# Kernel optimization log

Hardware: AMD Instinct MI355X
Metric: run time of the kernel (lower is better)

## Reference

```python
import jax, jax.numpy as jnp
import numpy as np
import math

EPS = 1e-6
NUM_HEADS = 8


def _layernorm(x, g, b):
    mu = jnp.mean(x, axis=-1, keepdims=True)
    var = jnp.mean(jnp.square(x - mu), axis=-1, keepdims=True)
    return (x - mu) * jax.lax.rsqrt(var + EPS) * g + b


def _pos_embed(n, d):
    pos = jnp.arange(n, dtype=jnp.float32)[:, None]                  # [N,1]
    div = jnp.exp(jnp.arange(0, d, 2, dtype=jnp.float32) * (-math.log(10000.0) / d))
    ang = pos * div                                                  # [N,d/2]
    pe = jnp.stack([jnp.sin(ang), jnp.cos(ang)], axis=-1).reshape(n, d)
    return pe


def setup_inputs() -> dict:
    key = jax.random.key(0)
    B, N, C, L = 2, 2048, 256, 4
    ks = jax.random.split(key, 6)
    s = 0.02
    return {
        "x": jax.random.normal(ks[0], (B, N, C), jnp.float32),
        "qkv_w": jax.random.normal(ks[1], (L, C, 3 * C), jnp.float32) * s,
        "proj_w": jax.random.normal(ks[2], (L, C, C), jnp.float32) * s,
        "proj_b": jnp.zeros((L, C), jnp.float32),
        "w1": jax.random.normal(ks[3], (L, C, C), jnp.float32) * s,
        "b1": jnp.zeros((L, C), jnp.float32),
        "w2": jax.random.normal(ks[4], (L, C, C), jnp.float32) * s,
        "b2": jnp.zeros((L, C), jnp.float32),
        "g1": jnp.ones((L, C), jnp.float32),
        "be1": jnp.zeros((L, C), jnp.float32),
        "g2": jnp.ones((L, C), jnp.float32),
        "be2": jnp.zeros((L, C), jnp.float32),
    }


def reference(x, qkv_w, proj_w, proj_b, w1, b1, w2, b2, g1, be1, g2, be2):
    B, N, C = x.shape
    L = qkv_w.shape[0]
    H = NUM_HEADS
    dh = C // H
    scale = dh ** -0.5

    x = x + _pos_embed(N, C)[None]

    for l in range(L):
        # --- attention (manual QKV, post-norm residual as in source) ---
        qkv = (x @ qkv_w[l]).reshape(B, N, 3, H, dh)
        q, k, v = qkv[:, :, 0], qkv[:, :, 1], qkv[:, :, 2]           # [B,N,H,dh]
        attn = jnp.einsum('bqhd,bkhd->bhqk', q, k) * scale           # [B,H,N,N]
        attn = jax.nn.softmax(attn, axis=-1)
        o = jnp.einsum('bhqk,bkhd->bqhd', attn, v).reshape(B, N, C)
        o = o @ proj_w[l] + proj_b[l]
        x = _layernorm(x + o, g1[l], be1[l])
        # --- MLP (GELU exact, as torch nn.GELU default) ---
        m = jax.nn.gelu(x @ w1[l] + b1[l], approximate=False) @ w2[l] + b2[l]
        x = _layernorm(x + m, g2[l], be2[l])
    return x
```

## Files before the change

kernel.cpp:

```cpp
#include <hip/hip_runtime.h>
#include <math.h>

#define Bd 2
#define Nd 2048
#define Cd 256
#define Ld 4
#define Hd 8
#define Md (Bd*Nd)
#define BHd 16
#define U32d 1024
#define SPLITd 4

typedef __attribute__((ext_vector_type(8))) short bf16x8;
typedef __attribute__((ext_vector_type(4))) float f32x4;
typedef __attribute__((ext_vector_type(16))) float f32x16;
typedef __attribute__((ext_vector_type(4))) short shortx4;

static __device__ inline f32x4 mfma16(bf16x8 a, bf16x8 b, f32x4 c) {
    return __builtin_amdgcn_mfma_f32_16x16x32_bf16(a, b, c, 0, 0, 0);
}
static __device__ inline f32x16 mfma32(bf16x8 a, bf16x8 b, f32x16 c) {
    return __builtin_amdgcn_mfma_f32_32x32x16_bf16(a, b, c, 0, 0, 0);
}
static __device__ inline short f2bf(float f) {
    union { float f; unsigned u; } v; v.f = f;
    unsigned r = (v.u + 0x7fff + ((v.u >> 16) & 1)) >> 16;
    return (short)r;
}
static __device__ inline unsigned pkbf(float a, float b) {
    unsigned r;
    asm("v_cvt_pk_bf16_f32 %0, %1, %2" : "=v"(r) : "v"(a), "v"(b));
    return r;
}
static __device__ inline float bf2f(unsigned u) {
    return __uint_as_float((u & 0xffffu) << 16);
}

__global__ __launch_bounds__(256)
void prep_kernel(const float* __restrict__ x_in, const float* __restrict__ qkv_w,
                 const float* __restrict__ proj_w, const float* __restrict__ w1,
                 const float* __restrict__ w2, float* __restrict__ xf,
                 short* __restrict__ xb, short* __restrict__ qkvT,
                 short* __restrict__ projT, short* __restrict__ w1T,
                 short* __restrict__ w2T, float qscale)
{
    __shared__ float tile[32][33];
    int id = blockIdx.x;
    if (id < 1536) {
        const float* src; short* dst; int Nc; float scale; int lim; int rem; int l;
        if (id < 768)       { l = id / 192;         rem = id % 192; src = qkv_w;  dst = qkvT;  Nc = 768; scale = qscale; lim = 256; }
        else if (id < 1024) { l = (id - 768) / 64;  rem = (id - 768) % 64;  src = proj_w; dst = projT; Nc = 256; scale = 1.f; lim = 0; }
        else if (id < 1280) { l = (id - 1024) / 64; rem = (id - 1024) % 64; src = w1;     dst = w1T;   Nc = 256; scale = 1.f; lim = 0; }
        else                { l = (id - 1280) / 64; rem = (id - 1280) % 64; src = w2;     dst = w2T;   Nc = 256; scale = 1.f; lim = 0; }
        int nb = Nc >> 5;
        int c0 = (rem % nb) * 32, k0 = (rem / nb) * 32;
        src += (size_t)l * 256 * Nc;
        dst += (size_t)l * Nc * 256;
        int tx = threadIdx.x & 31, ty = threadIdx.x >> 5;
#pragma unroll
        for (int i = 0; i < 4; i++) {
            int k = ty + 8 * i;
            tile[k][tx] = src[(size_t)(k0 + k) * Nc + c0 + tx];
        }
        __syncthreads();
#pragma unroll
        for (int i = 0; i < 4; i++) {
            int cc = ty + 8 * i;
            int col = c0 + cc;
            float v = tile[tx][cc];
            if (col < lim) v *= scale;
            dst[(size_t)col * 256 + k0 + tx] = f2bf(v);
        }
    } else {
        int i = (id - 1536) * 256 + threadIdx.x;
        int c = i & (Cd - 1);
        int n = (i >> 8) & (Nd - 1);
        const float kneg = -9.210340371976184f / 256.0f;
        float div = __expf((float)(c & ~1) * kneg);
        float ang = (float)n * div;
        float pe = (c & 1) ? cosf(ang) : sinf(ang);
        float v = x_in[i] + pe;
        xf[i] = v;
        xb[i] = f2bf(v);
    }
}

__global__ __launch_bounds__(256)
void qkv_gemm_kernel(const short* __restrict__ Ab, const short* __restrict__ WT,
                     short* __restrict__ Qh, short* __restrict__ Kh,
                     short* __restrict__ Vtb)
{
    int t = threadIdx.x, w = t >> 6, l = t & 63, c = l & 15, g = l >> 4;
    int rowBase = blockIdx.y * 128 + w * 32;
    int colBase = blockIdx.x * 32;
    const f32x4 zero = {0.f, 0.f, 0.f, 0.f};
    f32x4 acc[2][2] = {{zero, zero}, {zero, zero}};
    const short* ap0 = Ab + (size_t)(rowBase + c) * 256 + g * 8;
    const short* ap1 = ap0 + 16 * 256;
    const short* bp0 = WT + (size_t)(colBase + c) * 256 + g * 8;
    const short* bp1 = bp0 + 16 * 256;
#pragma unroll
    for (int kc = 0; kc < 256; kc += 32) {
        bf16x8 a0 = *(const bf16x8*)(ap0 + kc);
        bf16x8 a1 = *(const bf16x8*)(ap1 + kc);
        bf16x8 b0 = *(const bf16x8*)(bp0 + kc);
        bf16x8 b1 = *(const bf16x8*)(bp1 + kc);
        acc[0][0] = mfma16(a0, b0, acc[0][0]);
        acc[0][1] = mfma16(a0, b1, acc[0][1]);
        acc[1][0] = mfma16(a1, b0, acc[1][0]);
        acc[1][1] = mfma16(a1, b1, acc[1][1]);
    }
    int region = colBase >> 8;
    if (region < 2) {
        short* dst = (region == 0) ? Qh : Kh;
        int cb = colBase - region * 256;
#pragma unroll
        for (int m = 0; m < 2; m++)
#pragma unroll
            for (int n = 0; n < 2; n++) {
                int col = cb + 16 * n + c;
                int h = col >> 5, dh = col & 31;
#pragma unroll
                for (int r = 0; r < 4; r++) {
                    int tok = rowBase + 16 * m + 4 * g + r;
                    int b = tok >> 11, nt = tok & (Nd - 1);
                    dst[((size_t)(b * Hd + h) * Nd + nt) * 32 + dh] = f2bf(acc[m][n][r]);
                }
            }
    } else {
        int b = rowBase >> 11;
        int ntok0 = (rowBase & (Nd - 1)) + 4 * g;
#pragma unroll
        for (int m = 0; m < 2; m++)
#pragma unroll
            for (int n = 0; n < 2; n++) {
                int chg = colBase - 512 + 16 * n + c;
                shortx4 pkv;
#pragma unroll
                for (int r = 0; r < 4; r++) pkv[r] = f2bf(acc[m][n][r]);
                *(shortx4*)&Vtb[(size_t)((b * Hd + (chg >> 5)) * 32 + (chg & 31)) * Nd
                                + ntok0 + 16 * m] = pkv;
            }
    }
}

__global__ __launch_bounds__(512)
void attn_part_kernel(const short* __restrict__ Qh, const short* __restrict__ Kh,
                      const short* __restrict__ Vtb, unsigned* __restrict__ OPb,
                      float* __restrict__ Lsum)
{
    __shared__ short Ks[2][128 * 40];
    __shared__ short Vs[2][32 * 136];

    int t = threadIdx.x, w = t >> 6, l = t & 63;
    int l5 = l >> 5, q32 = l & 31;
    int bid = blockIdx.x;
    int xcd = bid & 7, j = bid >> 3;
    int grp = xcd * 8 + (j >> 3);
    int qt = (j & 7) * 8 + w;
    int part = grp >> 4, bh = grp & 15;

    bool isK = (t < 256);
    int t2 = t & 255;
    int koff = (t2 >> 1) * 40 + (t2 & 1) * 16;
    int voff = (t2 >> 3) * 136 + (t2 & 7) * 16;
    int soff = isK ? koff : voff;
    long sstep = isK ? 128 * 32 : 128;

    const int kstart = part * (Nd / SPLITd);
    const short* sg = isK
        ? Kh + ((size_t)bh * Nd + kstart + (t2 >> 1)) * 32 + (t2 & 1) * 16
        : Vtb + ((size_t)bh * 32 + (t2 >> 3)) * Nd + kstart + (t2 & 7) * 16;

    bf16x8 qf0, qf1;
    {
        const short* qp = Qh + ((size_t)bh * Nd + qt * 32 + q32) * 32 + 8 * l5;
        qf0 = *(const bf16x8*)qp;
        qf1 = *(const bf16x8*)(qp + 16);
    }

    f32x16 O;
#pragma unroll
    for (int i = 0; i < 16; i++) O[i] = 0.f;
    float lsum = 0.f;

    {
        bf16x8 r0 = *(const bf16x8*)sg;
        bf16x8 r1 = *(const bf16x8*)(sg + 8);
        short* d = (isK ? Ks[0] : Vs[0]) + soff;
        *(bf16x8*)d = r0;
        *(bf16x8*)(d + 8) = r1;
    }
    __syncthreads();

    const int NT = (Nd / SPLITd) / 128;
    int cur = 0;
    for (int it = 0; it < NT; ++it) {
        bool has_next = (it + 1) < NT;
        bf16x8 nxt0, nxt1;
        if (has_next) {
            sg += sstep;
            nxt0 = *(const bf16x8*)sg;
            nxt1 = *(const bf16x8*)(sg + 8);
        }

        __builtin_amdgcn_s_setprio(1);
#pragma unroll
        for (int sb = 0; sb < 4; sb++) {
            bf16x8 kf0 = *(const bf16x8*)&Ks[cur][(32 * sb + q32) * 40 + 8 * l5];
            bf16x8 kf1 = *(const bf16x8*)&Ks[cur][(32 * sb + q32) * 40 + 8 * l5 + 16];
            f32x16 s;
#pragma unroll
            for (int i = 0; i < 16; i++) s[i] = 0.f;
            s = mfma32(kf0, qf0, s);
            s = mfma32(kf1, qf1, s);
            float e[16];
#pragma unroll
            for (int i = 0; i < 16; i++) e[i] = exp2f(s[i]);
            float p0 = e[0] + e[1],  p1 = e[2] + e[3];
            float p2 = e[4] + e[5],  p3 = e[6] + e[7];
            float p4 = e[8] + e[9],  p5 = e[10] + e[11];
            float p6 = e[12] + e[13], p7 = e[14] + e[15];
            p0 += p1; p2 += p3; p4 += p5; p6 += p7;
            p0 += p2; p4 += p6;
            lsum += p0 + p4;
            unsigned wd[8];
#pragma unroll
            for (int i = 0; i < 8; i++) wd[i] = pkbf(e[2 * i], e[2 * i + 1]);
#pragma unroll
            for (int half = 0; half < 2; half++) {
                unsigned a0 = wd[4 * half], a1 = wd[4 * half + 1];
                unsigned b0 = wd[4 * half + 2], b1 = wd[4 * half + 3];
                asm("v_permlane32_swap_b32 %0, %1" : "+v"(a0), "+v"(b0));
                asm("v_permlane32_swap_b32 %0, %1" : "+v"(a1), "+v"(b1));
                union { unsigned u[4]; bf16x8 v; } pa;
                pa.u[0] = a0; pa.u[1] = a1; pa.u[2] = b0; pa.u[3] = b1;
                bf16x8 vvf = *(const bf16x8*)&Vs[cur][q32 * 136 + 8 * l5 + 16 * (2 * sb + half)];
                O = mfma32(pa.v, vvf, O);
            }
        }
        __builtin_amdgcn_s_setprio(0);

        if (has_next) {
            short* d = (isK ? Ks[cur ^ 1] : Vs[cur ^ 1]) + soff;
            *(bf16x8*)d = nxt0;
            *(bf16x8*)(d + 8) = nxt1;
            __syncthreads();
            cur ^= 1;
        }
    }

    lsum += __shfl_xor(lsum, 32, 64);

    int u = bh * 64 + qt;
    unsigned* opb = OPb + ((size_t)part * U32d + u) * 512;
#pragma unroll
    for (int i = 0; i < 16; i += 2) {
        int q = (i & 3) + 8 * (i >> 2) + 4 * l5;
        opb[(q >> 1) * 32 + q32] = pkbf(O[i], O[i + 1]);
    }
    if (l5 == 0) Lsum[((size_t)part * U32d + u) * 32 + q32] = lsum;
}

template<int LAST>
__global__ __launch_bounds__(512)
void tail_kernel(const unsigned* __restrict__ OPb, const float* __restrict__ Lsum,
                 const short* __restrict__ WT, const float* __restrict__ bias,
                 const float* __restrict__ resid,
                 const float* __restrict__ g1v, const float* __restrict__ be1v,
                 const short* __restrict__ W1T, const float* __restrict__ b1v,
                 const short* __restrict__ W2T, const float* __restrict__ b2v,
                 const float* __restrict__ g2v, const float* __restrict__ be2v,
                 float* __restrict__ outf, short* __restrict__ outb)
{
    __shared__ short Atile[16 * 264];
    __shared__ short A1[16 * 264];
    __shared__ short A2[16 * 264];
    __shared__ float red[8][16][2];
    int t = threadIdx.x;
    int rowBase = blockIdx.x * 16;

    {
        int r = t >> 5, seg = t & 31;
        int grow = rowBase + r;
        int bb = grow >> 11;
        int qt = (grow & (Nd - 1)) >> 5;
        int q = grow & 31;
        int h = seg >> 2;
        int dh0 = (seg & 3) * 8;
        int u = (bb * Hd + h) * 64 + qt;
        int sh = (q & 1) * 16;
        float o[8] = {0.f, 0.f, 0.f, 0.f, 0.f, 0.f, 0.f, 0.f};
        float L = 0.f;
#pragma unroll
        for (int p = 0; p < SPLITd; p++) {
            const unsigned* src = OPb + ((size_t)p * U32d + u) * 512 + (q >> 1) * 32 + dh0;
            uint4 w0 = *(const uint4*)src;
            uint4 w1 = *(const uint4*)(src + 4);
            o[0] += bf2f(w0.x >> sh); o[1] += bf2f(w0.y >> sh);
            o[2] += bf2f(w0.z >> sh); o[3] += bf2f(w0.w >> sh);
            o[4] += bf2f(w1.x >> sh); o[5] += bf2f(w1.y >> sh);
            o[6] += bf2f(w1.z >> sh); o[7] += bf2f(w1.w >> sh);
            L += Lsum[((size_t)p * U32d + u) * 32 + q];
        }
        float inv = 1.f / L;
        bf16x8 pk;
#pragma unroll
        for (int j = 0; j < 8; j++) pk[j] = f2bf(o[j] * inv);
        *(bf16x8*)&Atile[r * 264 + seg * 8] = pk;
    }
    __syncthreads();

    int w = t >> 6, l = t & 63, c = l & 15, g = l >> 4;
    const f32x4 zero = {0.f, 0.f, 0.f, 0.f};
    int col0 = w * 32 + c, col1 = col0 + 16;

    f32x4 acc0 = zero, acc1 = zero;
    {
        const short* bp0 = WT + (size_t)col0 * 256 + g * 8;
        const short* bp1 = WT + (size_t)col1 * 256 + g * 8;
#pragma unroll
        for (int kc = 0; kc < 256; kc += 32) {
            bf16x8 a = *(const bf16x8*)&Atile[c * 264 + g * 8 + kc];
            acc0 = mfma16(a, *(const bf16x8*)(bp0 + kc), acc0);
            acc1 = mfma16(a, *(const bf16x8*)(bp1 + kc), acc1);
        }
    }

    float vv[2][4], s_[4] = {0.f, 0.f, 0.f, 0.f}, sq_[4] = {0.f, 0.f, 0.f, 0.f};
    {
        float bi0 = bias[col0], bi1 = bias[col1];
#pragma unroll
        for (int r = 0; r < 4; r++) {
            int row = rowBase + 4 * g + r;
            float v0 = acc0[r] + bi0 + resid[(size_t)row * 256 + col0];
            float v1 = acc1[r] + bi1 + resid[(size_t)row * 256 + col1];
            vv[0][r] = v0; vv[1][r] = v1;
            s_[r] += v0 + v1; sq_[r] += v0 * v0 + v1 * v1;
        }
    }
#pragma unroll
    for (int off = 1; off <= 8; off <<= 1)
#pragma unroll
        for (int r = 0; r < 4; r++) {
            s_[r] += __shfl_xor(s_[r], off, 64);
            sq_[r] += __shfl_xor(sq_[r], off, 64);
        }
    if (c == 0)
#pragma unroll
        for (int r = 0; r < 4; r++) {
            red[w][4 * g + r][0] = s_[r];
            red[w][4 * g + r][1] = sq_[r];
        }
    __syncthreads();
    float ln1[2][4];
    {
        float mu[4], rs[4];
#pragma unroll
        for (int r = 0; r < 4; r++) {
            float S = 0.f, Q = 0.f;
#pragma unroll
            for (int ww = 0; ww < 8; ww++) { S += red[ww][4 * g + r][0]; Q += red[ww][4 * g + r][1]; }
            mu[r] = S * (1.f / 256.f);
            rs[r] = rsqrtf(Q * (1.f / 256.f) - mu[r] * mu[r] + 1e-6f);
        }
        float gv0 = g1v[col0], bv0 = be1v[col0], gv1 = g1v[col1], bv1 = be1v[col1];
#pragma unroll
        for (int r = 0; r < 4; r++) {
            float o0 = (vv[0][r] - mu[r]) * rs[r] * gv0 + bv0;
            float o1 = (vv[1][r] - mu[r]) * rs[r] * gv1 + bv1;
            ln1[0][r] = o0; ln1[1][r] = o1;
            A1[(4 * g + r) * 264 + col0] = f2bf(o0);
            A1[(4 * g + r) * 264 + col1] = f2bf(o1);
        }
    }
    __syncthreads();

    {
        f32x4 a0 = zero, a1 = zero;
        const short* bp0 = W1T + (size_t)col0 * 256 + g * 8;
        const short* bp1 = W1T + (size_t)col1 * 256 + g * 8;
#pragma unroll
        for (int kc = 0; kc < 256; kc += 32) {
            bf16x8 a = *(const bf16x8*)&A1[c * 264 + g * 8 + kc];
            a0 = mfma16(a, *(const bf16x8*)(bp0 + kc), a0);
            a1 = mfma16(a, *(const bf16x8*)(bp1 + kc), a1);
        }
        float bi0 = b1v[col0], bi1 = b1v[col1];
#pragma unroll
        for (int r = 0; r < 4; r++) {
            float v0 = a0[r] + bi0, v1 = a1[r] + bi1;
            v0 = 0.5f * v0 * (1.f + erff(v0 * 0.7071067811865476f));
            v1 = 0.5f * v1 * (1.f + erff(v1 * 0.7071067811865476f));
            A2[(4 * g + r) * 264 + col0] = f2bf(v0);
            A2[(4 * g + r) * 264 + col1] = f2bf(v1);
        }
    }
    __syncthreads();

    acc0 = zero; acc1 = zero;
    {
        const short* bp0 = W2T + (size_t)col0 * 256 + g * 8;
        const short* bp1 = W2T + (size_t)col1 * 256 + g * 8;
#pragma unroll
        for (int kc = 0; kc < 256; kc += 32) {
            bf16x8 a = *(const bf16x8*)&A2[c * 264 + g * 8 + kc];
            acc0 = mfma16(a, *(const bf16x8*)(bp0 + kc), acc0);
            acc1 = mfma16(a, *(const bf16x8*)(bp1 + kc), acc1);
        }
    }
    {
        float bi0 = b2v[col0], bi1 = b2v[col1];
        float t0[4] = {0.f, 0.f, 0.f, 0.f}, t1[4] = {0.f, 0.f, 0.f, 0.f};
#pragma unroll
        for (int r = 0; r < 4; r++) {
            float v0 = acc0[r] + bi0 + ln1[0][r];
            float v1 = acc1[r] + bi1 + ln1[1][r];
            vv[0][r] = v0; vv[1][r] = v1;
            t0[r] = v0 + v1; t1[r] = v0 * v0 + v1 * v1;
        }
#pragma unroll
        for (int off = 1; off <= 8; off <<= 1)
#pragma unroll
            for (int r = 0; r < 4; r++) {
                t0[r] += __shfl_xor(t0[r], off, 64);
                t1[r] += __shfl_xor(t1[r], off, 64);
            }
        if (c == 0)
#pragma unroll
            for (int r = 0; r < 4; r++) {
                red[w][4 * g + r][0] = t0[r];
                red[w][4 * g + r][1] = t1[r];
            }
    }
    __syncthreads();
    {
        float mu[4], rs[4];
#pragma unroll
        for (int r = 0; r < 4; r++) {
            float S = 0.f, Q = 0.f;
#pragma unroll
            for (int ww = 0; ww < 8; ww++) { S += red[ww][4 * g + r][0]; Q += red[ww][4 * g + r][1]; }
            mu[r] = S * (1.f / 256.f);
            rs[r] = rsqrtf(Q * (1.f / 256.f) - mu[r] * mu[r] + 1e-6f);
        }
        float gv0 = g2v[col0], bv0 = be2v[col0], gv1 = g2v[col1], bv1 = be2v[col1];
#pragma unroll
        for (int r = 0; r < 4; r++) {
            int row = rowBase + 4 * g + r;
            float o0 = (vv[0][r] - mu[r]) * rs[r] * gv0 + bv0;
            float o1 = (vv[1][r] - mu[r]) * rs[r] * gv1 + bv1;
            outf[(size_t)row * 256 + col0] = o0;
            outf[(size_t)row * 256 + col1] = o1;
            if (!LAST) {
                outb[(size_t)row * 256 + col0] = f2bf(o0);
                outb[(size_t)row * 256 + col1] = f2bf(o1);
            }
        }
    }
}

extern "C" void kernel_launch(void* const* d_in, const int* in_sizes, int n_in,
                              void* d_out, int out_size, void* d_ws, size_t ws_size,
                              hipStream_t stream)
{
    const float* x_in   = (const float*)d_in[0];
    const float* qkv_w  = (const float*)d_in[1];
    const float* proj_w = (const float*)d_in[2];
    const float* proj_b = (const float*)d_in[3];
    const float* w1     = (const float*)d_in[4];
    const float* b1     = (const float*)d_in[5];
    const float* w2     = (const float*)d_in[6];
    const float* b2     = (const float*)d_in[7];
    const float* g1     = (const float*)d_in[8];
    const float* be1    = (const float*)d_in[9];
    const float* g2     = (const float*)d_in[10];
    const float* be2    = (const float*)d_in[11];
    float* outp = (float*)d_out;

    char* p = (char*)d_ws;
    float* xf    = (float*)p;    p += (size_t)Md * Cd * 4;
    short* xb    = (short*)p;    p += (size_t)Md * Cd * 2;
    short* Qh    = (short*)p;    p += (size_t)Md * Cd * 2;
    short* Kh    = (short*)p;    p += (size_t)Md * Cd * 2;
    short* Vtb   = (short*)p;    p += (size_t)Md * Cd * 2;
    unsigned* OPb = (unsigned*)p; p += (size_t)SPLITd * U32d * 512 * 4;
    float* Lsum  = (float*)p;    p += (size_t)SPLITd * U32d * 32 * 4;
    short* qkvT  = (short*)p;    p += (size_t)Ld * 768 * 256 * 2;
    short* projT = (short*)p;    p += (size_t)Ld * 256 * 256 * 2;
    short* w1T   = (short*)p;    p += (size_t)Ld * 256 * 256 * 2;
    short* w2T   = (short*)p;    p += (size_t)Ld * 256 * 256 * 2;

    const float QSCALE = 0.17677669529663687f * 1.4426950408889634f;
    prep_kernel<<<1536 + Md * Cd / 256, 256, 0, stream>>>(
        x_in, qkv_w, proj_w, w1, w2, xf, xb, qkvT, projT, w1T, w2T, QSCALE);

    for (int l = 0; l < Ld; l++) {
        qkv_gemm_kernel<<<dim3(24, 32), 256, 0, stream>>>(
            xb, qkvT + (size_t)l * 768 * 256, Qh, Kh, Vtb);
        attn_part_kernel<<<512, 512, 0, stream>>>(Qh, Kh, Vtb, OPb, Lsum);
        if (l == Ld - 1)
            tail_kernel<1><<<Md / 16, 512, 0, stream>>>(
                OPb, Lsum, projT + (size_t)l * 65536, proj_b + l * 256, xf,
                g1 + l * 256, be1 + l * 256,
                w1T + (size_t)l * 65536, b1 + l * 256,
                w2T + (size_t)l * 65536, b2 + l * 256,
                g2 + l * 256, be2 + l * 256, outp, nullptr);
        else
            tail_kernel<0><<<Md / 16, 512, 0, stream>>>(
                OPb, Lsum, projT + (size_t)l * 65536, proj_b + l * 256, xf,
                g1 + l * 256, be1 + l * 256,
                w1T + (size_t)l * 65536, b1 + l * 256,
                w2T + (size_t)l * 65536, b2 + l * 256,
                g2 + l * 256, be2 + l * 256, xf, xb);
    }
}
```

Before: 302.3 us.

## Double attention key split and read K fragments directly from global memory

Raises the key-dimension split from 4 to 8 parts and doubles the attention grid to 1024 blocks, so more workgroups run over shorter key ranges. K is no longer staged in shared memory: each lane loads its K fragments straight from global memory (through cache), and only V stays double-buffered in LDS. This cuts LDS usage and the cooperative K staging work, but adds redundant global K reads across waves plus twice the partial outputs and sums for the tail kernel to combine. The tail kernel's handling of SPLITd in hidden code must match.

Result: slower. 315.1 us (+4.2%).

```diff
diff --git a/kernel.cpp b/kernel.cpp
--- a/kernel.cpp
+++ b/kernel.cpp
@@ -9,7 +9,7 @@
 #define Md (Bd*Nd)
 #define BHd 16
 #define U32d 1024
-#define SPLITd 4
+#define SPLITd 8
 
 typedef __attribute__((ext_vector_type(8))) short bf16x8;
 typedef __attribute__((ext_vector_type(4))) float f32x4;
@@ -149,28 +149,22 @@
                       const short* __restrict__ Vtb, unsigned* __restrict__ OPb,
                       float* __restrict__ Lsum)
 {
-    __shared__ short Ks[2][128 * 40];
     __shared__ short Vs[2][32 * 136];
 
     int t = threadIdx.x, w = t >> 6, l = t & 63;
     int l5 = l >> 5, q32 = l & 31;
     int bid = blockIdx.x;
     int xcd = bid & 7, j = bid >> 3;
-    int grp = xcd * 8 + (j >> 3);
+    int grp = xcd * 16 + (j >> 3);
     int qt = (j & 7) * 8 + w;
     int part = grp >> 4, bh = grp & 15;
 
-    bool isK = (t < 256);
-    int t2 = t & 255;
-    int koff = (t2 >> 1) * 40 + (t2 & 1) * 16;
-    int voff = (t2 >> 3) * 136 + (t2 & 7) * 16;
-    int soff = isK ? koff : voff;
-    long sstep = isK ? 128 * 32 : 128;
+    int vdh = t >> 4, vk = (t & 15) * 8;
+    int voff = vdh * 136 + vk;
 
     const int kstart = part * (Nd / SPLITd);
-    const short* sg = isK
-        ? Kh + ((size_t)bh * Nd + kstart + (t2 >> 1)) * 32 + (t2 & 1) * 16
-        : Vtb + ((size_t)bh * 32 + (t2 >> 3)) * Nd + kstart + (t2 & 7) * 16;
+    const short* vg = Vtb + ((size_t)bh * 32 + vdh) * Nd + kstart + vk;
+    const short* kbase = Kh + (size_t)bh * Nd * 32 + 8 * l5;
 
     bf16x8 qf0, qf1;
     {
@@ -185,11 +179,8 @@
     float lsum = 0.f;
 
     {
-        bf16x8 r0 = *(const bf16x8*)sg;
-        bf16x8 r1 = *(const bf16x8*)(sg + 8);
-        short* d = (isK ? Ks[0] : Vs[0]) + soff;
-        *(bf16x8*)d = r0;
-        *(bf16x8*)(d + 8) = r1;
+        bf16x8 r0 = *(const bf16x8*)vg;
+        *(bf16x8*)&Vs[0][voff] = r0;
     }
     __syncthreads();
 
@@ -197,18 +188,19 @@
     int cur = 0;
     for (int it = 0; it < NT; ++it) {
         bool has_next = (it + 1) < NT;
-        bf16x8 nxt0, nxt1;
+        bf16x8 vnxt;
         if (has_next) {
-            sg += sstep;
-            nxt0 = *(const bf16x8*)sg;
-            nxt1 = *(const bf16x8*)(sg + 8);
+            vg += 128;
+            vnxt = *(const bf16x8*)vg;
         }
 
         __builtin_amdgcn_s_setprio(1);
 #pragma unroll
         for (int sb = 0; sb < 4; sb++) {
-            bf16x8 kf0 = *(const bf16x8*)&Ks[cur][(32 * sb + q32) * 40 + 8 * l5];
-            bf16x8 kf1 = *(const bf16x8*)&Ks[cur][(32 * sb + q32) * 40 + 8 * l5 + 16];
+            int key = kstart + it * 128 + sb * 32 + q32;
+            const short* kp = kbase + (size_t)key * 32;
+            bf16x8 kf0 = *(const bf16x8*)kp;
+            bf16x8 kf1 = *(const bf16x8*)(kp + 16);
             f32x16 s;
 #pragma unroll
             for (int i = 0; i < 16; i++) s[i] = 0.f;
@@ -242,9 +234,7 @@
         __builtin_amdgcn_s_setprio(0);
 
         if (has_next) {
-            short* d = (isK ? Ks[cur ^ 1] : Vs[cur ^ 1]) + soff;
-            *(bf16x8*)d = nxt0;
-            *(bf16x8*)(d + 8) = nxt1;
+            *(bf16x8*)&Vs[cur ^ 1][voff] = vnxt;
             __syncthreads();
             cur ^= 1;
         }
@@ -498,7 +488,7 @@
     for (int l = 0; l < Ld; l++) {
         qkv_gemm_kernel<<<dim3(24, 32), 256, 0, stream>>>(
             xb, qkvT + (size_t)l * 768 * 256, Qh, Kh, Vtb);
-        attn_part_kernel<<<512, 512, 0, stream>>>(Qh, Kh, Vtb, OPb, Lsum);
+        attn_part_kernel<<<1024, 512, 0, stream>>>(Qh, Kh, Vtb, OPb, Lsum);
         if (l == Ld - 1)
             tail_kernel<1><<<Md / 16, 512, 0, stream>>>(
                 OPb, Lsum, projT + (size_t)l * 65536, proj_b + l * 256, xf,
```
